# Optimization experiments

Hardware: AMD Instinct MI355X
Metric: run time of the kernel (lower is better)

The kernel has to match this reference:

```python
import jax, jax.numpy as jnp
import numpy as np


def _pool2(t):
    # 2x2 max-pool + 2x2 avg-pool, summed. t: [B, C, H, W] with even H, W
    B, C, H, W = t.shape
    r = t.reshape(B, C, H // 2, 2, W // 2, 2)
    return r.max(axis=(3, 5)) + r.mean(axis=(3, 5))


def setup_inputs() -> dict:
    key = jax.random.key(0)
    k1, k2, k3, k4 = jax.random.split(key, 4)
    B, C, H, W = 32, 256, 56, 56
    x = jax.random.normal(k1, (B, C, H, W), dtype=jnp.float32)
    W1 = jax.random.normal(k2, (C // 2, C), dtype=jnp.float32) * 0.05
    W2 = jax.random.normal(k3, (C // 2, C), dtype=jnp.float32) * 0.05
    W3 = jax.random.normal(k4, (C, C), dtype=jnp.float32) * 0.05
    gamma = jnp.zeros((1,), dtype=jnp.float32)
    return {"x": x, "W1": W1, "W2": W2, "W3": W3, "gamma": gamma}


def reference(x, W1, W2, W3, gamma):
    B, C, H, W = x.shape
    # 1x1 convs (bias-free) == channel matmuls
    c1 = jnp.einsum('oc,bchw->bohw', W1, x)  # [B, C/2, H, W]
    c2 = jnp.einsum('oc,bchw->bohw', W2, x)  # [B, C/2, H, W]
    c3 = jnp.einsum('oc,bchw->bohw', W3, x)  # [B, C,   H, W]
    c1p = _pool2(c1)  # [B, C/2, H/2, W/2]
    c3p = _pool2(c3)  # [B, C,   H/2, W/2]
    n = H * W
    m = n // 4
    c1p_f = c1p.reshape(B, C // 2, m)
    c2_f = c2.reshape(B, C // 2, n)
    c3p_f = c3p.reshape(B, C, m)
    # matrix[b, n, m] = sum_c c2[b,c,n] * c1p[b,c,m]
    matrix = jnp.einsum('bcn,bcm->bnm', c2_f, c1p_f)
    attention = jax.nn.softmax(matrix, axis=-1)  # [B, n, m]
    # refined[b, c, n] = sum_m c3p[b,c,m] * attention[b,n,m]
    refined = jnp.einsum('bcm,bnm->bcn', c3p_f, attention).reshape(B, C, H, W)
    return gamma[0] * refined + x
```

## Files before the change

kernel.cpp:

```cpp
#include <hip/hip_runtime.h>

#define BATCH 32
#define CIN   256
#define CHALF 128
#define NPIX  3136
#define MPOOL 784
#define MPAD  896

typedef __bf16 bf16;
typedef __bf16 bf16x2 __attribute__((ext_vector_type(2)));
typedef __bf16 bf16x4 __attribute__((ext_vector_type(4)));
typedef __bf16 bf16x8 __attribute__((ext_vector_type(8)));
typedef float  f32x4  __attribute__((ext_vector_type(4)));

__global__ __launch_bounds__(256) void k_cast(
    const float* __restrict__ W1, const float* __restrict__ W2,
    const float* __restrict__ W3, bf16* __restrict__ WcatF)
{
    int u = blockIdx.x * 256 + threadIdx.x;
    int lane = u & 63, frag = u >> 6;
    int ks = frag & 7, ot = frag >> 3;
    int o = ot * 16 + (lane & 15);
    int c0 = ks * 32 + (lane >> 4) * 8;
    const float* src = (o < 128) ? (W1 + o * 256)
                     : (o < 256) ? (W2 + (o - 128) * 256)
                                 : (W3 + (o - 256) * 256);
    float4 v0 = *(const float4*)(src + c0);
    float4 v1 = *(const float4*)(src + c0 + 4);
    bf16x8 w = { (bf16)v0.x, (bf16)v0.y, (bf16)v0.z, (bf16)v0.w,
                 (bf16)v1.x, (bf16)v1.y, (bf16)v1.z, (bf16)v1.w };
    *(bf16x8*)(WcatF + (size_t)u * 8) = w;
}

#define XS_STRIDE   528
#define SLAB_STRIDE 520

__global__ __launch_bounds__(512) void k_conv(
    const float* __restrict__ x, const bf16* __restrict__ WcatF,
    bf16* __restrict__ c2n, bf16* __restrict__ c1pT, bf16* __restrict__ c3p)
{
    const int h2 = blockIdx.x, b = blockIdx.y;
    const int t = threadIdx.x;
    const int lane = t & 63, wave = t >> 6;
    const int l15 = lane & 15, lg = lane >> 4;

    __shared__ __align__(16) unsigned char smem[59136];

    if (h2 == 0) {
        float4 z = {0.f, 0.f, 0.f, 0.f};
        float4* p1 = (float4*)(c1pT + (size_t)b * MPAD * CHALF + (size_t)MPOOL * CHALF);
        for (int u = t; u < 1792; u += 512) p1[u] = z;
        bf16* p3 = c3p + (size_t)b * CIN * MPAD + MPOOL;
        for (int u = t; u < 256 * 14; u += 512) {
            int c = u / 14, g = u % 14;
            *(float4*)((char*)(p3 + (size_t)c * MPAD) + g * 16) = z;
        }
    }

    {
        const float* xb = x + (size_t)b * CIN * NPIX + h2 * 112;
        float vv[14][4];
        #pragma unroll
        for (int i = 0; i < 14; ++i) {
            int u = t + i * 512;
            int c4 = u / 112, n = u - c4 * 112;
            const float* s = xb + (size_t)(c4 * 4) * NPIX + n;
            vv[i][0] = s[0];
            vv[i][1] = s[NPIX];
            vv[i][2] = s[2 * NPIX];
            vv[i][3] = s[3 * NPIX];
        }
        #pragma unroll
        for (int i = 0; i < 14; ++i) {
            int u = t + i * 512;
            int c4 = u / 112, n = u - c4 * 112;
            bf16x4 w = {(bf16)vv[i][0], (bf16)vv[i][1], (bf16)vv[i][2], (bf16)vv[i][3]};
            *(bf16x4*)(smem + n * XS_STRIDE + c4 * 8) = w;
        }
    }
    __syncthreads();

    f32x4 acc[4][7];
    #pragma unroll
    for (int fo = 0; fo < 4; ++fo)
        #pragma unroll
        for (int fn = 0; fn < 7; ++fn) {
            f32x4 zz = {0.f, 0.f, 0.f, 0.f};
            acc[fo][fn] = zz;
        }
    {
        const unsigned char* xsb = smem + l15 * XS_STRIDE + lg * 16;
        const bf16* wfb = WcatF + (((size_t)wave * 4) * 8 + 0) * 64 * 8 + (size_t)lane * 8;
        #pragma unroll
        for (int ks = 0; ks < 8; ++ks) {
            bf16x8 afr[4], bfr[7];
            #pragma unroll
            for (int fo = 0; fo < 4; ++fo)
                afr[fo] = *(const bf16x8*)(wfb + (size_t)(fo * 8 + ks) * 64 * 8);
            #pragma unroll
            for (int fn = 0; fn < 7; ++fn)
                bfr[fn] = *(const bf16x8*)(xsb + fn * 16 * XS_STRIDE + ks * 64);
            #pragma unroll
            for (int fo = 0; fo < 4; ++fo)
                #pragma unroll
                for (int fn = 0; fn < 7; ++fn)
                    acc[fo][fn] = __builtin_amdgcn_mfma_f32_16x16x32_bf16(
                        afr[fo], bfr[fn], acc[fo][fn], 0, 0, 0);
        }
    }

    __syncthreads();
    if (wave < 4) {
        #pragma unroll
        for (int fo = 0; fo < 4; ++fo)
            #pragma unroll
            for (int fn = 0; fn < 7; ++fn) {
                int n = fn * 16 + l15;
                int ol = wave * 64 + fo * 16 + lg * 4;
                f32x4 a = acc[fo][fn];
                bf16x4 w = {(bf16)a[0], (bf16)a[1], (bf16)a[2], (bf16)a[3]};
                *(bf16x4*)(smem + n * SLAB_STRIDE + ol * 2) = w;
            }
    }
    __syncthreads();
    {
        bf16* dst = c1pT + (size_t)b * MPAD * CHALF + (size_t)h2 * 28 * CHALF;
        for (int u = t; u < 896; u += 512) {
            int w2 = u >> 5, o4 = (u & 31) * 4;
            bf16x4 r0 = *(bf16x4*)(smem + (2 * w2)      * SLAB_STRIDE + o4 * 2);
            bf16x4 r1 = *(bf16x4*)(smem + (2 * w2 + 1)  * SLAB_STRIDE + o4 * 2);
            bf16x4 r2 = *(bf16x4*)(smem + (56 + 2 * w2) * SLAB_STRIDE + o4 * 2);
            bf16x4 r3 = *(bf16x4*)(smem + (57 + 2 * w2) * SLAB_STRIDE + o4 * 2);
            bf16x4 o_;
            #pragma unroll
            for (int j = 0; j < 4; ++j) {
                float p0 = (float)r0[j], p1 = (float)r1[j];
                float p2 = (float)r2[j], p3 = (float)r3[j];
                float mx = fmaxf(fmaxf(p0, p1), fmaxf(p2, p3));
                float av = (p0 + p1 + p2 + p3) * 0.25f;
                o_[j] = (bf16)(mx + av);
            }
            *(bf16x4*)(dst + (size_t)w2 * CHALF + o4) = o_;
        }
    }
    {
        bf16* dst = c2n + (size_t)b * NPIX * CHALF + (size_t)h2 * 112 * CHALF;
        for (int u = t; u < 3584; u += 512) {
            int n = u >> 5, o4 = (u & 31) * 4;
            bf16x4 v = *(bf16x4*)(smem + n * SLAB_STRIDE + 256 + o4 * 2);
            *(bf16x4*)(dst + (size_t)n * CHALF + o4) = v;
        }
    }

    __syncthreads();
    if (wave >= 4) {
        #pragma unroll
        for (int fo = 0; fo < 4; ++fo)
            #pragma unroll
            for (int fn = 0; fn < 7; ++fn) {
                int n = fn * 16 + l15;
                int ol = (wave - 4) * 64 + fo * 16 + lg * 4;
                f32x4 a = acc[fo][fn];
                bf16x4 w = {(bf16)a[0], (bf16)a[1], (bf16)a[2], (bf16)a[3]};
                *(bf16x4*)(smem + n * SLAB_STRIDE + ol * 2) = w;
            }
    }
    __syncthreads();
    {
        bf16* dst = c3p + (size_t)b * CIN * MPAD + h2 * 28;
        for (int u = t; u < 3584; u += 512) {
            int c = u / 14, w2p = u - c * 14;
            bf16x2 o_;
            #pragma unroll
            for (int k = 0; k < 2; ++k) {
                int w2 = 2 * w2p + k;
                float p0 = (float)*(bf16*)(smem + (2 * w2)      * SLAB_STRIDE + c * 2);
                float p1 = (float)*(bf16*)(smem + (2 * w2 + 1)  * SLAB_STRIDE + c * 2);
                float p2 = (float)*(bf16*)(smem + (56 + 2 * w2) * SLAB_STRIDE + c * 2);
                float p3 = (float)*(bf16*)(smem + (57 + 2 * w2) * SLAB_STRIDE + c * 2);
                float mx = fmaxf(fmaxf(p0, p1), fmaxf(p2, p3));
                float av = (p0 + p1 + p2 + p3) * 0.25f;
                o_[k] = (bf16)(mx + av);
            }
            *(bf16x2*)(dst + (size_t)c * MPAD + 2 * w2p) = o_;
        }
    }
}

#define STG_OFF 114688

__global__ __launch_bounds__(512) void k_attn(
    const bf16* __restrict__ c2n,
    const bf16* __restrict__ c1pT,
    const bf16* __restrict__ c3p,
    const float* __restrict__ x,
    const float* __restrict__ gamma,
    float* __restrict__ out)
{
    const int orig = blockIdx.x;
    const int wid = (orig & 7) * 196 + (orig >> 3);
    const int b = wid / 49, nb = wid % 49;
    const int n0 = nb * 64;
    const int t = threadIdx.x;
    const int lane = t & 63, wave = t >> 6;
    const int l15 = lane & 15, lg = lane >> 4;
    const int p = wave & 3, h = wave >> 2;

    __shared__ __align__(16) unsigned char smem[147456];
    unsigned char* stg = smem + STG_OFF;
    float* EX = (float*)stg;

    bf16x8 bq[4];
    {
        const bf16* c2b = c2n + ((size_t)b * NPIX + n0 + p * 16 + l15) * CHALF + lg * 8;
        #pragma unroll
        for (int k = 0; k < 4; ++k) bq[k] = *(const bf16x8*)(c2b + k * 32);
    }
    const bf16* c1b = c1pT + (size_t)b * MPAD * CHALF;
    const bf16* c3b = c3p + (size_t)b * CIN * MPAD;

    const int r0 = t >> 4, s0 = t & 15;
    const int cs = (s0 & 8) | ((s0 & 7) ^ (r0 & 7));
    const bf16* sA = c1b + (size_t)r0 * CHALF + cs * 8;
    const bf16* sB = c1b + (size_t)(448 + r0) * CHALF + cs * 8;

    uint4 rXa, rXb, rYa, rYb;
    rXa = *(const uint4*)(sA);
    rXb = *(const uint4*)(sB);
    *(uint4*)(stg + t * 16) = rXa;
    *(uint4*)(stg + 8192 + t * 16) = rXb;
    rYa = *(const uint4*)(sA + 4096);
    rYb = *(const uint4*)(sB + 4096);
    __syncthreads();

    f32x4 sacc[28];
    #pragma unroll
    for (int j = 0; j < 28; ++j) {
        f32x4 z = {0.f, 0.f, 0.f, 0.f};
        sacc[j] = z;
    }

    #pragma unroll
    for (int mc = 0; mc < 14; ++mc) {
        const unsigned char* bufc = stg + (mc & 1) * 16384;
        unsigned char* bufn = stg + ((mc & 1) ^ 1) * 16384;
        if (mc + 1 < 14) {
            if (mc & 1) { *(uint4*)(bufn + t * 16) = rXa; *(uint4*)(bufn + 8192 + t * 16) = rXb; }
            else        { *(uint4*)(bufn + t * 16) = rYa; *(uint4*)(bufn + 8192 + t * 16) = rYb; }
        }
        if (mc + 2 < 14) {
            if (mc & 1) { rYa = *(const uint4*)(sA + (mc + 2) * 4096); rYb = *(const uint4*)(sB + (mc + 2) * 4096); }
            else        { rXa = *(const uint4*)(sA + (mc + 2) * 4096); rXb = *(const uint4*)(sB + (mc + 2) * 4096); }
        }
        #pragma unroll
        for (int sf = 0; sf < 2; ++sf) {
            bf16x8 af[4];
            #pragma unroll
            for (int k = 0; k < 4; ++k)
                af[k] = *(const bf16x8*)(bufc + h * 8192 + (sf * 16 + l15) * 256
                                         + ((lg * 16 + k * 64) ^ ((l15 & 7) << 4)));
            #pragma unroll
            for (int k = 0; k < 4; ++k)
                sacc[mc * 2 + sf] = __builtin_amdgcn_mfma_f32_16x16x32_bf16(
                    af[k], bq[k], sacc[mc * 2 + sf], 0, 0, 0);
        }
        __syncthreads();
    }

    float mx = -1e30f;
    #pragma unroll
    for (int j = 0; j < 28; ++j) {
        if (h == 0 || j < 21)
            mx = fmaxf(mx, fmaxf(fmaxf(sacc[j][0], sacc[j][1]),
                                 fmaxf(sacc[j][2], sacc[j][3])));
    }
    mx = fmaxf(mx, __shfl_xor(mx, 16));
    mx = fmaxf(mx, __shfl_xor(mx, 32));
    if (lane < 16) EX[wave * 16 + l15] = mx;
    __syncthreads();
    mx = fmaxf(mx, EX[(wave ^ 4) * 16 + l15]);

    float s = 0.f;
    #pragma unroll
    for (int j = 0; j < 28; ++j) {
        if (h == 0 || j < 21) {
            #pragma unroll
            for (int r = 0; r < 4; ++r) {
                float e = __expf(sacc[j][r] - mx);
                sacc[j][r] = e;
                s += e;
            }
        }
    }
    s += __shfl_xor(s, 16);
    s += __shfl_xor(s, 32);
    if (lane < 16) EX[128 + wave * 16 + l15] = s;
    __syncthreads();
    s += EX[128 + (wave ^ 4) * 16 + l15];
    const float ri = 1.f / s;

    const int pc = t >> 2, ps = t & 3;
    const bf16* sV  = c3b + (size_t)pc * MPAD + ((ps ^ ((pc >> 1) & 3)) * 8);
    const bf16* sV2 = c3b + (size_t)(pc + 128) * MPAD + ((ps ^ ((pc >> 1) & 3)) * 8);
    rXa = *(const uint4*)(sV);
    rXb = *(const uint4*)(sV2);

    {
        const int n = p * 16 + l15;
        const unsigned sw = (unsigned)((n & 7) << 4);
        const unsigned rowb = (unsigned)(n * 1792);
        #pragma unroll
        for (int j = 0; j < 28; ++j) {
            bf16x4 w;
            if (h == 0 || j < 21) {
                w = bf16x4{ (bf16)(sacc[j][0] * ri), (bf16)(sacc[j][1] * ri),
                            (bf16)(sacc[j][2] * ri), (bf16)(sacc[j][3] * ri) };
            } else {
                w = bf16x4{ (bf16)0.f, (bf16)0.f, (bf16)0.f, (bf16)0.f };
            }
            unsigned byte = rowb + (unsigned)(h * 896 + j * 32 + lg * 8);
            *(bf16x4*)(smem + (byte ^ sw)) = w;
        }
    }
    __syncthreads();

    *(uint4*)(stg + t * 16) = rXa;
    *(uint4*)(stg + 8192 + t * 16) = rXb;
    rYa = *(const uint4*)(sV + 32);
    rYb = *(const uint4*)(sV2 + 32);
    __syncthreads();

    const int wn = h, wq = p;
    f32x4 acc2[2][4];
    #pragma unroll
    for (int fn = 0; fn < 2; ++fn)
        #pragma unroll
        for (int fc = 0; fc < 4; ++fc) {
            f32x4 z = {0.f, 0.f, 0.f, 0.f};
            acc2[fn][fc] = z;
        }

    #pragma unroll
    for (int ks = 0; ks < 28; ++ks) {
        const unsigned char* bufc = stg + (ks & 1) * 16384;
        unsigned char* bufn = stg + ((ks & 1) ^ 1) * 16384;
        if (ks + 1 < 28) {
            if (ks & 1) { *(uint4*)(bufn + t * 16) = rXa; *(uint4*)(bufn + 8192 + t * 16) = rXb; }
            else        { *(uint4*)(bufn + t * 16) = rYa; *(uint4*)(bufn + 8192 + t * 16) = rYb; }
        }
        if (ks + 2 < 28) {
            if (ks & 1) { rYa = *(const uint4*)(sV + (ks + 2) * 32); rYb = *(const uint4*)(sV2 + (ks + 2) * 32); }
            else        { rXa = *(const uint4*)(sV + (ks + 2) * 32); rXb = *(const uint4*)(sV2 + (ks + 2) * 32); }
        }
        {
            int nA0 = wn * 32 + l15, nA1 = nA0 + 16;
            int mb = (ks * 32 + lg * 8) * 2;
            bf16x8 af0 = *(const bf16x8*)(smem + ((nA0 * 1792 + mb) ^ ((nA0 & 7) << 4)));
            bf16x8 af1 = *(const bf16x8*)(smem + ((nA1 * 1792 + mb) ^ ((nA1 & 7) << 4)));
            #pragma unroll
            for (int fc = 0; fc < 4; ++fc) {
                int c = wq * 64 + fc * 16 + l15;
                bf16x8 bfr = *(const bf16x8*)(bufc + c * 64 + ((lg ^ ((c >> 1) & 3)) * 16));
                acc2[0][fc] = __builtin_amdgcn_mfma_f32_16x16x32_bf16(af0, bfr, acc2[0][fc], 0, 0, 0);
                acc2[1][fc] = __builtin_amdgcn_mfma_f32_16x16x32_bf16(af1, bfr, acc2[1][fc], 0, 0, 0);
            }
        }
        __syncthreads();
    }

    float* R = (float*)smem;
    #pragma unroll
    for (int fn = 0; fn < 2; ++fn)
        #pragma unroll
        for (int fc = 0; fc < 4; ++fc) {
            int c = wq * 64 + fc * 16 + l15;
            #pragma unroll
            for (int r = 0; r < 4; ++r) {
                int n = wn * 32 + fn * 16 + lg * 4 + r;
                R[n * 257 + c] = acc2[fn][fc][r];
            }
        }
    __syncthreads();
    const float g = gamma[0];
    const float* xb = x + (size_t)b * CIN * NPIX + n0;
    float* ob = out + (size_t)b * CIN * NPIX + n0;
    #pragma unroll 4
    for (int i = 0; i < 32; ++i) {
        int idx = t + i * 512;
        int c = idx >> 6, nn = idx & 63;
        size_t off = (size_t)c * NPIX + nn;
        ob[off] = g * R[nn * 257 + c] + xb[off];
    }
}

extern "C" void kernel_launch(void* const* d_in, const int* in_sizes, int n_in,
                              void* d_out, int out_size, void* d_ws, size_t ws_size,
                              hipStream_t stream) {
    const float* x     = (const float*)d_in[0];
    const float* W1    = (const float*)d_in[1];
    const float* W2    = (const float*)d_in[2];
    const float* W3    = (const float*)d_in[3];
    const float* gamma = (const float*)d_in[4];
    float* out = (float*)d_out;

    bf16* ws    = (bf16*)d_ws;
    bf16* WcatF = ws;
    bf16* c2n   = WcatF + (size_t)512 * 256;
    bf16* c1pT  = c2n + (size_t)BATCH * NPIX * CHALF;
    bf16* c3p   = c1pT + (size_t)BATCH * MPAD * CHALF;

    k_cast<<<64, 256, 0, stream>>>(W1, W2, W3, WcatF);
    k_conv<<<dim3(28, BATCH), 512, 0, stream>>>(x, WcatF, c2n, c1pT, c3p);
    k_attn<<<1568, 512, 0, stream>>>(c2n, c1pT, c3p, x, gamma, out);
}
```

Baseline: 243.3 us.

## Halve attention query tile to 32 rows for two blocks per CU

Each k_attn block now handles 32 query pixels instead of 64, with the 8 waves split across the key dimension (4 m-slices) instead of two halves. This cuts per-block shared memory from 144KB to about 73KB and registers for the score accumulators, allowing two blocks per CU via launch bounds. The grid becomes 98x32 with a simple 2D mapping, the XCD-aware block remapping is dropped, and the PV stage switches to a single-buffered V stage with two barriers per step. The cost is re-reading the K/V tiles twice as often per output pixel and extra syncs in the PV loop.

New measurement: 294.7 us. 1.21x slower.

```diff
diff --git a/kernel.cpp b/kernel.cpp
--- a/kernel.cpp
+++ b/kernel.cpp
@@ -187,9 +187,9 @@
     }
 }
 
-#define STG_OFF 114688
-
-__global__ __launch_bounds__(512) void k_attn(
+#define PVSTG 57344
+
+__global__ __launch_bounds__(512, 2) void k_attn(
     const bf16* __restrict__ c2n,
     const bf16* __restrict__ c1pT,
     const bf16* __restrict__ c3p,
@@ -197,18 +197,18 @@
     const float* __restrict__ gamma,
     float* __restrict__ out)
 {
-    const int orig = blockIdx.x;
-    const int wid = (orig & 7) * 196 + (orig >> 3);
-    const int b = wid / 49, nb = wid % 49;
-    const int n0 = nb * 64;
+    const int nb = blockIdx.x, b = blockIdx.y;
+    const int n0 = nb * 32;
     const int t = threadIdx.x;
     const int lane = t & 63, wave = t >> 6;
     const int l15 = lane & 15, lg = lane >> 4;
-    const int p = wave & 3, h = wave >> 2;
-
-    __shared__ __align__(16) unsigned char smem[147456];
-    unsigned char* stg = smem + STG_OFF;
-    float* EX = (float*)stg;
+    const int p = wave & 1, ms = wave >> 1;
+
+    __shared__ __align__(16) unsigned char smem[74752];
+    unsigned char* stg0 = smem;
+    unsigned char* stg1 = smem + 16384;
+    unsigned char* vstg = smem + PVSTG;
+    float* EX = (float*)(smem + PVSTG + 16384);
 
     bf16x8 bq[4];
     {
@@ -222,55 +222,53 @@
     const int r0 = t >> 4, s0 = t & 15;
     const int cs = (s0 & 8) | ((s0 & 7) ^ (r0 & 7));
     const bf16* sA = c1b + (size_t)r0 * CHALF + cs * 8;
-    const bf16* sB = c1b + (size_t)(448 + r0) * CHALF + cs * 8;
+    const bf16* sB = c1b + (size_t)(32 + r0) * CHALF + cs * 8;
 
     uint4 rXa, rXb, rYa, rYb;
     rXa = *(const uint4*)(sA);
     rXb = *(const uint4*)(sB);
-    *(uint4*)(stg + t * 16) = rXa;
-    *(uint4*)(stg + 8192 + t * 16) = rXb;
-    rYa = *(const uint4*)(sA + 4096);
-    rYb = *(const uint4*)(sB + 4096);
-    __syncthreads();
-
-    f32x4 sacc[28];
-    #pragma unroll
-    for (int j = 0; j < 28; ++j) {
+    *(uint4*)(stg0 + t * 16) = rXa;
+    *(uint4*)(stg0 + 8192 + t * 16) = rXb;
+    rYa = *(const uint4*)(sA + 8192);
+    rYb = *(const uint4*)(sB + 8192);
+    __syncthreads();
+
+    f32x4 sacc[14];
+    #pragma unroll
+    for (int j = 0; j < 14; ++j) {
         f32x4 z = {0.f, 0.f, 0.f, 0.f};
         sacc[j] = z;
     }
 
     #pragma unroll
-    for (int mc = 0; mc < 14; ++mc) {
-        const unsigned char* bufc = stg + (mc & 1) * 16384;
-        unsigned char* bufn = stg + ((mc & 1) ^ 1) * 16384;
-        if (mc + 1 < 14) {
-            if (mc & 1) { *(uint4*)(bufn + t * 16) = rXa; *(uint4*)(bufn + 8192 + t * 16) = rXb; }
-            else        { *(uint4*)(bufn + t * 16) = rYa; *(uint4*)(bufn + 8192 + t * 16) = rYb; }
-        }
-        if (mc + 2 < 14) {
-            if (mc & 1) { rYa = *(const uint4*)(sA + (mc + 2) * 4096); rYb = *(const uint4*)(sB + (mc + 2) * 4096); }
-            else        { rXa = *(const uint4*)(sA + (mc + 2) * 4096); rXb = *(const uint4*)(sB + (mc + 2) * 4096); }
-        }
-        #pragma unroll
-        for (int sf = 0; sf < 2; ++sf) {
+    for (int j = 0; j < 14; ++j) {
+        const unsigned char* bufc = (j & 1) ? stg1 : stg0;
+        unsigned char* bufn = (j & 1) ? stg0 : stg1;
+        if (j + 1 < 14) {
+            if (j & 1) { *(uint4*)(bufn + t * 16) = rXa; *(uint4*)(bufn + 8192 + t * 16) = rXb; }
+            else       { *(uint4*)(bufn + t * 16) = rYa; *(uint4*)(bufn + 8192 + t * 16) = rYb; }
+        }
+        if (j + 2 < 14) {
+            if (j & 1) { rYa = *(const uint4*)(sA + (j + 2) * 8192); rYb = *(const uint4*)(sB + (j + 2) * 8192); }
+            else       { rXa = *(const uint4*)(sA + (j + 2) * 8192); rXb = *(const uint4*)(sB + (j + 2) * 8192); }
+        }
+        {
             bf16x8 af[4];
             #pragma unroll
             for (int k = 0; k < 4; ++k)
-                af[k] = *(const bf16x8*)(bufc + h * 8192 + (sf * 16 + l15) * 256
+                af[k] = *(const bf16x8*)(bufc + (ms * 16 + l15) * 256
                                          + ((lg * 16 + k * 64) ^ ((l15 & 7) << 4)));
             #pragma unroll
             for (int k = 0; k < 4; ++k)
-                sacc[mc * 2 + sf] = __builtin_amdgcn_mfma_f32_16x16x32_bf16(
-                    af[k], bq[k], sacc[mc * 2 + sf], 0, 0, 0);
+                sacc[j] = __builtin_amdgcn_mfma_f32_16x16x32_bf16(af[k], bq[k], sacc[j], 0, 0, 0);
         }
         __syncthreads();
     }
 
     float mx = -1e30f;
     #pragma unroll
-    for (int j = 0; j < 28; ++j) {
-        if (h == 0 || j < 21)
+    for (int j = 0; j < 14; ++j) {
+        if (j < 12 || (j == 12 && ms == 0))
             mx = fmaxf(mx, fmaxf(fmaxf(sacc[j][0], sacc[j][1]),
                                  fmaxf(sacc[j][2], sacc[j][3])));
     }
@@ -278,12 +276,15 @@
     mx = fmaxf(mx, __shfl_xor(mx, 32));
     if (lane < 16) EX[wave * 16 + l15] = mx;
     __syncthreads();
-    mx = fmaxf(mx, EX[(wave ^ 4) * 16 + l15]);
-
+    {
+        float m0 = EX[(p)     * 16 + l15], m1 = EX[(2 + p) * 16 + l15];
+        float m2 = EX[(4 + p) * 16 + l15], m3 = EX[(6 + p) * 16 + l15];
+        mx = fmaxf(fmaxf(m0, m1), fmaxf(m2, m3));
+    }
     float s = 0.f;
     #pragma unroll
-    for (int j = 0; j < 28; ++j) {
-        if (h == 0 || j < 21) {
+    for (int j = 0; j < 14; ++j) {
+        if (j < 12 || (j == 12 && ms == 0)) {
             #pragma unroll
             for (int r = 0; r < 4; ++r) {
                 float e = __expf(sacc[j][r] - mx);
@@ -296,7 +297,11 @@
     s += __shfl_xor(s, 32);
     if (lane < 16) EX[128 + wave * 16 + l15] = s;
     __syncthreads();
-    s += EX[128 + (wave ^ 4) * 16 + l15];
+    {
+        float s0v = EX[128 + (p)     * 16 + l15], s1v = EX[128 + (2 + p) * 16 + l15];
+        float s2v = EX[128 + (4 + p) * 16 + l15], s3v = EX[128 + (6 + p) * 16 + l15];
+        s = (s0v + s1v) + (s2v + s3v);
+    }
     const float ri = 1.f / s;
 
     const int pc = t >> 2, ps = t & 3;
@@ -310,84 +315,68 @@
         const unsigned sw = (unsigned)((n & 7) << 4);
         const unsigned rowb = (unsigned)(n * 1792);
         #pragma unroll
-        for (int j = 0; j < 28; ++j) {
+        for (int j = 0; j < 14; ++j) {
             bf16x4 w;
-            if (h == 0 || j < 21) {
+            if (j < 12 || (j == 12 && ms == 0)) {
                 w = bf16x4{ (bf16)(sacc[j][0] * ri), (bf16)(sacc[j][1] * ri),
                             (bf16)(sacc[j][2] * ri), (bf16)(sacc[j][3] * ri) };
             } else {
                 w = bf16x4{ (bf16)0.f, (bf16)0.f, (bf16)0.f, (bf16)0.f };
             }
-            unsigned byte = rowb + (unsigned)(h * 896 + j * 32 + lg * 8);
+            unsigned byte = rowb + (unsigned)(j * 128 + ms * 32 + lg * 8);
             *(bf16x4*)(smem + (byte ^ sw)) = w;
         }
     }
-    __syncthreads();
-
-    *(uint4*)(stg + t * 16) = rXa;
-    *(uint4*)(stg + 8192 + t * 16) = rXb;
-    rYa = *(const uint4*)(sV + 32);
-    rYb = *(const uint4*)(sV2 + 32);
-    __syncthreads();
-
-    const int wn = h, wq = p;
-    f32x4 acc2[2][4];
-    #pragma unroll
-    for (int fn = 0; fn < 2; ++fn)
-        #pragma unroll
-        for (int fc = 0; fc < 4; ++fc) {
-            f32x4 z = {0.f, 0.f, 0.f, 0.f};
-            acc2[fn][fc] = z;
-        }
+
+    const int wq = wave >> 1, nd = wave & 1;
+    f32x4 acc2[4];
+    #pragma unroll
+    for (int fc = 0; fc < 4; ++fc) {
+        f32x4 z = {0.f, 0.f, 0.f, 0.f};
+        acc2[fc] = z;
+    }
+    const int nA = nd * 16 + l15;
+    const unsigned swA = (unsigned)((nA & 7) << 4);
+    const unsigned rbA = (unsigned)(nA * 1792);
 
     #pragma unroll
     for (int ks = 0; ks < 28; ++ks) {
-        const unsigned char* bufc = stg + (ks & 1) * 16384;
-        unsigned char* bufn = stg + ((ks & 1) ^ 1) * 16384;
+        __syncthreads();
+        *(uint4*)(vstg + t * 16) = (ks & 1) ? rYa : rXa;
+        *(uint4*)(vstg + 8192 + t * 16) = (ks & 1) ? rYb : rXb;
         if (ks + 1 < 28) {
-            if (ks & 1) { *(uint4*)(bufn + t * 16) = rXa; *(uint4*)(bufn + 8192 + t * 16) = rXb; }
-            else        { *(uint4*)(bufn + t * 16) = rYa; *(uint4*)(bufn + 8192 + t * 16) = rYb; }
-        }
-        if (ks + 2 < 28) {
-            if (ks & 1) { rYa = *(const uint4*)(sV + (ks + 2) * 32); rYb = *(const uint4*)(sV2 + (ks + 2) * 32); }
-            else        { rXa = *(const uint4*)(sV + (ks + 2) * 32); rXb = *(const uint4*)(sV2 + (ks + 2) * 32); }
-        }
+            if (ks & 1) { rXa = *(const uint4*)(sV + (ks + 1) * 32); rXb = *(const uint4*)(sV2 + (ks + 1) * 32); }
+            else        { rYa = *(const uint4*)(sV + (ks + 1) * 32); rYb = *(const uint4*)(sV2 + (ks + 1) * 32); }
+        }
+        __syncthreads();
         {
-            int nA0 = wn * 32 + l15, nA1 = nA0 + 16;
-            int mb = (ks * 32 + lg * 8) * 2;
-            bf16x8 af0 = *(const bf16x8*)(smem + ((nA0 * 1792 + mb) ^ ((nA0 & 7) << 4)));
-            bf16x8 af1 = *(const bf16x8*)(smem + ((nA1 * 1792 + mb) ^ ((nA1 & 7) << 4)));
+            bf16x8 af = *(const bf16x8*)(smem + ((rbA + (unsigned)(ks * 64 + lg * 16)) ^ swA));
             #pragma unroll
             for (int fc = 0; fc < 4; ++fc) {
                 int c = wq * 64 + fc * 16 + l15;
-                bf16x8 bfr = *(const bf16x8*)(bufc + c * 64 + ((lg ^ ((c >> 1) & 3)) * 16));
-                acc2[0][fc] = __builtin_amdgcn_mfma_f32_16x16x32_bf16(af0, bfr, acc2[0][fc], 0, 0, 0);
-                acc2[1][fc] = __builtin_amdgcn_mfma_f32_16x16x32_bf16(af1, bfr, acc2[1][fc], 0, 0, 0);
-            }
-        }
-        __syncthreads();
-    }
-
+                bf16x8 bfr = *(const bf16x8*)(vstg + c * 64 + ((lg ^ ((c >> 1) & 3)) * 16));
+                acc2[fc] = __builtin_amdgcn_mfma_f32_16x16x32_bf16(af, bfr, acc2[fc], 0, 0, 0);
+            }
+        }
+    }
+
+    __syncthreads();
     float* R = (float*)smem;
     #pragma unroll
-    for (int fn = 0; fn < 2; ++fn)
-        #pragma unroll
-        for (int fc = 0; fc < 4; ++fc) {
-            int c = wq * 64 + fc * 16 + l15;
-            #pragma unroll
-            for (int r = 0; r < 4; ++r) {
-                int n = wn * 32 + fn * 16 + lg * 4 + r;
-                R[n * 257 + c] = acc2[fn][fc][r];
-            }
-        }
+    for (int fc = 0; fc < 4; ++fc) {
+        int c = wq * 64 + fc * 16 + lg * 4;
+        #pragma unroll
+        for (int r = 0; r < 4; ++r)
+            R[(nd * 16 + l15) * 257 + c + r] = acc2[fc][r];
+    }
     __syncthreads();
     const float g = gamma[0];
     const float* xb = x + (size_t)b * CIN * NPIX + n0;
     float* ob = out + (size_t)b * CIN * NPIX + n0;
     #pragma unroll 4
-    for (int i = 0; i < 32; ++i) {
+    for (int i = 0; i < 16; ++i) {
         int idx = t + i * 512;
-        int c = idx >> 6, nn = idx & 63;
+        int c = idx >> 5, nn = idx & 31;
         size_t off = (size_t)c * NPIX + nn;
         ob[off] = g * R[nn * 257 + c] + xb[off];
     }
@@ -411,5 +400,5 @@
 
     k_cast<<<64, 256, 0, stream>>>(W1, W2, W3, WcatF);
     k_conv<<<dim3(28, BATCH), 512, 0, stream>>>(x, WcatF, c2n, c1pT, c3p);
-    k_attn<<<1568, 512, 0, stream>>>(c2n, c1pT, c3p, x, gamma, out);
+    k_attn<<<dim3(98, BATCH), 512, 0, stream>>>(c2n, c1pT, c3p, x, gamma, out);
 }
```
